# Performance work log

Measured on AMD Instinct MI355X. Metric: run time of the kernel, lower is better.

## Reference

```python
import jax, jax.numpy as jnp
import numpy as np

D_MODEL = 1024
H = 16
D_K = D_MODEL // H
B, S = 4, 2048
NEG = -1000000000.0


def setup_inputs() -> dict:
    key = jax.random.key(0)
    ks = jax.random.split(key, 12)
    scale = 1.0 / np.sqrt(D_MODEL)
    inp = {
        "query": jax.random.normal(ks[0], (B, S, D_MODEL), jnp.float32),
        "key": jax.random.normal(ks[1], (B, S, D_MODEL), jnp.float32),
        "value": jax.random.normal(ks[2], (B, S, D_MODEL), jnp.float32),
        # causal lower-triangular mask, shape (B, S, S); forward unsqueezes head dim
        "mask": jnp.broadcast_to(jnp.tril(jnp.ones((S, S), jnp.int32)), (B, S, S)),
        "Wq": jax.random.normal(ks[3], (D_MODEL, D_MODEL), jnp.float32) * scale,
        "bq": jnp.zeros((D_MODEL,), jnp.float32),
        "Wk": jax.random.normal(ks[4], (D_MODEL, D_MODEL), jnp.float32) * scale,
        "bk": jnp.zeros((D_MODEL,), jnp.float32),
        "Wv": jax.random.normal(ks[5], (D_MODEL, D_MODEL), jnp.float32) * scale,
        "bv": jnp.zeros((D_MODEL,), jnp.float32),
        "Wo": jax.random.normal(ks[6], (D_MODEL, D_MODEL), jnp.float32) * scale,
        "bo": jnp.zeros((D_MODEL,), jnp.float32),
    }
    return inp


def reference(query, key, value, mask, Wq, bq, Wk, bk, Wv, bv, Wo, bo):
    b, s, _ = query.shape
    # projections (torch Linear: x @ W.T + b); split into heads -> (b, h, s, d_k)
    def proj(x, W, bias):
        return (x @ W.T + bias).reshape(b, -1, H, D_K).transpose(0, 2, 1, 3)

    Q = proj(query, Wq, bq)
    K = proj(key, Wk, bk)
    V = proj(value, Wv, bv)

    scores = jnp.einsum("bhqd,bhkd->bhqk", Q, K) / np.sqrt(D_K)
    m = mask[:, None, :, :]  # (b, 1, s, s)
    scores = jnp.where(m == 0, NEG, scores)
    attn = jax.nn.softmax(scores, axis=-1)
    x = jnp.einsum("bhqk,bhkd->bhqd", attn, V)
    x = x.transpose(0, 2, 1, 3).reshape(b, -1, D_MODEL)
    return x @ Wo.T + bo
```

## Files before the change

### kernel.cpp

```cpp
#include <hip/hip_runtime.h>
#include <hip/hip_bf16.h>

#define DMODEL 1024
#define NH 16
#define DKH 64
#define NB 4
#define SEQ 2048
#define MTOT (NB*SEQ)

typedef __bf16 bf16_t;
typedef __bf16 bf16x8 __attribute__((ext_vector_type(8)));
typedef float f32x4 __attribute__((ext_vector_type(4)));

__device__ __forceinline__ void async_copy16(void* lds, const void* g) {
    __builtin_amdgcn_global_load_lds(
        (const __attribute__((address_space(1))) unsigned int*)g,
        (__attribute__((address_space(3))) unsigned int*)lds, 16, 0, 0);
}

__device__ __forceinline__ float fast_exp2(float x) {
    return __builtin_amdgcn_exp2f(x);
}

__device__ __forceinline__ float rsum16(float v) {
    v += __shfl_xor(v, 1);
    v += __shfl_xor(v, 2);
    v += __shfl_xor(v, 4);
    v += __shfl_xor(v, 8);
    return v;
}

__global__ void cvt_kernel(const float* __restrict__ s0, const float* __restrict__ s1,
                           const float* __restrict__ s2, const float* __restrict__ s3,
                           bf16_t* __restrict__ d0, bf16_t* __restrict__ d1,
                           bf16_t* __restrict__ d2, bf16_t* __restrict__ d3, int n)
{
    const float* s = (blockIdx.y == 0) ? s0 : (blockIdx.y == 1) ? s1 :
                     (blockIdx.y == 2) ? s2 : s3;
    bf16_t* d = (blockIdx.y == 0) ? d0 : (blockIdx.y == 1) ? d1 :
                (blockIdx.y == 2) ? d2 : d3;
    int i = (blockIdx.x * 256 + threadIdx.x) * 8;
    if (i < n) {
        float4 a = *(const float4*)&s[i];
        float4 b = *(const float4*)&s[i + 4];
        union { bf16_t h[8]; uint4 u; } t;
        t.h[0]=(bf16_t)a.x; t.h[1]=(bf16_t)a.y; t.h[2]=(bf16_t)a.z; t.h[3]=(bf16_t)a.w;
        t.h[4]=(bf16_t)b.x; t.h[5]=(bf16_t)b.y; t.h[6]=(bf16_t)b.z; t.h[7]=(bf16_t)b.w;
        *(uint4*)&d[i] = t.u;
    }
}

template<int OUT_MODE>
__global__ __launch_bounds__(256, 3)
void gemm_bt(const bf16_t* __restrict__ A, const bf16_t* __restrict__ W,
             const float* __restrict__ bias, void* __restrict__ out,
             int M, int N, int K, float scale)
{
    __shared__ bf16_t As[128 * 64];
    __shared__ bf16_t Ws[128 * 64];

    const int tid  = threadIdx.x;
    const int wave = tid >> 6;
    const int lane = tid & 63;
    const int ln   = lane & 15;
    const int quad = lane >> 4;
    const int wm   = (wave >> 1) * 64;
    const int wn   = (wave & 1) * 64;
    const int bm   = blockIdx.x * 128;
    const int bn   = blockIdx.y * 128;
    const int srow = wave * 8 + (lane >> 3);
    const int sg   = (lane & 7) * 8;

    f32x4 acc[4][4] = {};

    for (int k0 = 0; k0 < K; k0 += 64) {
        #pragma unroll
        for (int rr = 0; rr < 4; ++rr) {
            int row = rr * 32 + srow;
            async_copy16(&As[(size_t)(rr * 32 + wave * 8) * 64],
                         &A[(size_t)(bm + row) * K + k0 + sg]);
            async_copy16(&Ws[(size_t)(rr * 32 + wave * 8) * 64],
                         &W[(size_t)(bn + row) * K + k0 + sg]);
        }
        __syncthreads();

        bf16x8 af[2][4], wf[2][4];
        #pragma unroll
        for (int h = 0; h < 2; ++h)
            #pragma unroll
            for (int u = 0; u < 4; ++u) {
                af[h][u] = *(const bf16x8*)&As[(wm + u * 16 + ln) * 64 + h * 32 + quad * 8];
                wf[h][u] = *(const bf16x8*)&Ws[(wn + u * 16 + ln) * 64 + h * 32 + quad * 8];
            }
        #pragma unroll
        for (int h = 0; h < 2; ++h)
            #pragma unroll
            for (int im = 0; im < 4; ++im)
                #pragma unroll
                for (int jn = 0; jn < 4; ++jn)
                    acc[im][jn] = __builtin_amdgcn_mfma_f32_16x16x32_bf16(
                        af[h][im], wf[h][jn], acc[im][jn], 0, 0, 0);

        __syncthreads();
    }

    #pragma unroll
    for (int jn = 0; jn < 4; ++jn) {
        int n = bn + wn + jn * 16 + ln;
        float bv = bias[n];
        #pragma unroll
        for (int im = 0; im < 4; ++im) {
            #pragma unroll
            for (int r = 0; r < 4; ++r) {
                int m = bm + wm + im * 16 + quad * 4 + r;
                float v = (acc[im][jn][r] + bv) * scale;
                ((float*)out)[(size_t)m * N + n] = v;
            }
        }
    }
}

__global__ __launch_bounds__(256, 3)
void gemm_qkv(const bf16_t* __restrict__ Aq, const bf16_t* __restrict__ Ak,
              const bf16_t* __restrict__ Av, const bf16_t* __restrict__ W3,
              const float* __restrict__ bqp, const float* __restrict__ bkp,
              const float* __restrict__ bvp,
              bf16_t* __restrict__ Qh, bf16_t* __restrict__ Kh,
              bf16_t* __restrict__ Vth, float qscale)
{
    __shared__ bf16_t As[128 * 64];
    __shared__ bf16_t Ws[128 * 64];

    const int K    = DMODEL;
    const int tid  = threadIdx.x;
    const int wave = tid >> 6;
    const int lane = tid & 63;
    const int ln   = lane & 15;
    const int quad = lane >> 4;
    const int wm   = (wave >> 1) * 64;
    const int wn   = (wave & 1) * 64;
    const int bm   = blockIdx.x * 128;
    const int bnG  = blockIdx.y * 128;
    const int sel  = blockIdx.y >> 3;
    const bf16_t* A = (sel == 0) ? Aq : (sel == 1) ? Ak : Av;
    const int srow = wave * 8 + (lane >> 3);
    const int sg   = (lane & 7) * 8;

    f32x4 acc[4][4] = {};

    for (int k0 = 0; k0 < K; k0 += 64) {
        #pragma unroll
        for (int rr = 0; rr < 4; ++rr) {
            int row = rr * 32 + srow;
            async_copy16(&As[(size_t)(rr * 32 + wave * 8) * 64],
                         &A[(size_t)(bm + row) * K + k0 + sg]);
            async_copy16(&Ws[(size_t)(rr * 32 + wave * 8) * 64],
                         &W3[(size_t)(bnG + row) * K + k0 + sg]);
        }
        __syncthreads();

        bf16x8 af[2][4], wf[2][4];
        #pragma unroll
        for (int h = 0; h < 2; ++h)
            #pragma unroll
            for (int u = 0; u < 4; ++u) {
                af[h][u] = *(const bf16x8*)&As[(wm + u * 16 + ln) * 64 + h * 32 + quad * 8];
                wf[h][u] = *(const bf16x8*)&Ws[(wn + u * 16 + ln) * 64 + h * 32 + quad * 8];
            }
        #pragma unroll
        for (int h = 0; h < 2; ++h)
            #pragma unroll
            for (int im = 0; im < 4; ++im)
                #pragma unroll
                for (int jn = 0; jn < 4; ++jn)
                    acc[im][jn] = __builtin_amdgcn_mfma_f32_16x16x32_bf16(
                        af[h][im], wf[h][jn], acc[im][jn], 0, 0, 0);

        __syncthreads();
    }

    const float* bias = (sel == 0) ? bqp : (sel == 1) ? bkp : bvp;
    const float scale = (sel == 0) ? qscale : 1.0f;
    const int bn = bnG & (DMODEL - 1);

    #pragma unroll
    for (int jn = 0; jn < 4; ++jn) {
        int n = bn + wn + jn * 16 + ln;
        float bv = bias[n];
        int h = n >> 6, d = n & 63;
        #pragma unroll
        for (int im = 0; im < 4; ++im) {
            #pragma unroll
            for (int r = 0; r < 4; ++r) {
                int m = bm + wm + im * 16 + quad * 4 + r;
                float v = (acc[im][jn][r] + bv) * scale;
                int b = m >> 11, s = m & (SEQ - 1);
                if (sel == 2) {
                    Vth[(((size_t)(b * NH + h)) * DKH + d) * SEQ + s] = (bf16_t)v;
                } else {
                    bf16_t* outp = (sel == 1) ? Kh : Qh;
                    outp[(((size_t)(b * NH + h)) * SEQ + s) * DKH + d] = (bf16_t)v;
                }
            }
        }
    }
}

__global__ __launch_bounds__(256, 2)
void attn_kernel(const bf16_t* __restrict__ Q, const bf16_t* __restrict__ Km,
                 const bf16_t* __restrict__ Vt, bf16_t* __restrict__ X)
{
    __shared__ __align__(16) bf16_t Ks[2][64 * 64];
    __shared__ __align__(16) bf16_t Vs[2][64 * 64];
    __shared__ __align__(16) bf16_t Ps[4][32][72];

    const int tid  = threadIdx.x;
    const int wave = tid >> 6;
    const int lane = tid & 63;
    const int ln   = lane & 15;
    const int quad = lane >> 4;
    const int cs   = ln & 7;

    const int bh  = blockIdx.x;
    const int qtA = blockIdx.y;
    const int qtB = 15 - qtA;
    const int q0A = qtA * 128;
    const int q0B = qtB * 128;
    const size_t base = (size_t)bh * SEQ * DKH;

    bf16x8 aq[4][2];
    #pragma unroll
    for (int st = 0; st < 4; ++st) {
        const int sb = ((st < 2) ? q0A : q0B) + (st & 1) * 64;
        const bf16_t* qr = Q + base + (size_t)(sb + wave * 16 + ln) * DKH;
        aq[st][0] = *(const bf16x8*)(qr + quad * 8);
        aq[st][1] = *(const bf16x8*)(qr + 32 + quad * 8);
    }

    f32x4 oacc[4][4] = {};
    float psum[4][4] = {};

    const int nkt = 2 * qtB + 2;

    const int srow8 = lane >> 3;
    const int schk  = lane & 7;

    #pragma unroll
    for (int qq = 0; qq < 2; ++qq) {
        const int rb  = wave * 16 + qq * 8;
        const int row = rb + srow8;
        const int csr = schk ^ (row & 7);
        async_copy16(&Ks[0][rb * 64], Km + base + (size_t)row * DKH + csr * 8);
        async_copy16(&Vs[0][rb * 64], Vt + base + (size_t)row * SEQ + csr * 8);
    }
    __syncthreads();

    int cur = 0;
    for (int kt = 0; kt < nkt; ++kt, cur ^= 1) {
        const int j0 = kt * 64;

        if (kt + 1 < nkt) {
            const int jn0 = j0 + 64;
            #pragma unroll
            for (int qq = 0; qq < 2; ++qq) {
                const int rb  = wave * 16 + qq * 8;
                const int row = rb + srow8;
                const int csr = schk ^ (row & 7);
                async_copy16(&Ks[cur ^ 1][rb * 64],
                             Km + base + (size_t)(jn0 + row) * DKH + csr * 8);
                async_copy16(&Vs[cur ^ 1][rb * 64],
                             Vt + base + (size_t)row * SEQ + jn0 + csr * 8);
            }
        }

        bf16x8 kf[4][2];
        #pragma unroll
        for (int jn = 0; jn < 4; ++jn) {
            const int rr = (jn * 16 + ln) * 64;
            kf[jn][0] = *(const bf16x8*)&Ks[cur][rr + ((quad    ) ^ cs) * 8];
            kf[jn][1] = *(const bf16x8*)&Ks[cur][rr + ((4 + quad) ^ cs) * 8];
        }
        bf16x8 vf[4][2];
        #pragma unroll
        for (int nj = 0; nj < 4; ++nj) {
            const int rr = (nj * 16 + ln) * 64;
            vf[nj][0] = *(const bf16x8*)&Vs[cur][rr + ((quad    ) ^ cs) * 8];
            vf[nj][1] = *(const bf16x8*)&Vs[cur][rr + ((4 + quad) ^ cs) * 8];
        }

        #pragma unroll
        for (int pair = 0; pair < 2; ++pair) {
            const int q0p = (pair == 0) ? q0A : q0B;

            f32x4 s[2][4] = {};
            #pragma unroll
            for (int sl = 0; sl < 2; ++sl) {
                const int st = pair * 2 + sl;
                const int sb = q0p + sl * 64;
                if (j0 > sb + 63) continue;
                #pragma unroll
                for (int jn = 0; jn < 4; ++jn) {
                    s[sl][jn] = __builtin_amdgcn_mfma_f32_16x16x32_bf16(aq[st][0], kf[jn][0], s[sl][jn], 0, 0, 0);
                    s[sl][jn] = __builtin_amdgcn_mfma_f32_16x16x32_bf16(aq[st][1], kf[jn][1], s[sl][jn], 0, 0, 0);
                }
            }

            #pragma unroll
            for (int sl = 0; sl < 2; ++sl) {
                const int st = pair * 2 + sl;
                const int sb = q0p + sl * 64;
                if (j0 > sb + 63) continue;
                const int rbase = sb + wave * 16 + quad * 4;
                const bool diag = (j0 + 63 > sb);
                #pragma unroll
                for (int r = 0; r < 4; ++r) {
                    float rowsum = 0.f;
                    #pragma unroll
                    for (int jn = 0; jn < 4; ++jn) {
                        float v = s[sl][jn][r];
                        if (diag) {
                            int col = j0 + jn * 16 + ln;
                            if (col > rbase + r) v = -1e30f;
                        }
                        float p = fast_exp2(v);
                        s[sl][jn][r] = p;
                        rowsum += p;
                    }
                    psum[st][r] += rowsum;
                }
                #pragma unroll
                for (int r = 0; r < 4; ++r)
                    #pragma unroll
                    for (int jn = 0; jn < 4; ++jn)
                        Ps[wave][sl * 16 + quad * 4 + r][jn * 16 + ln] = (bf16_t)s[sl][jn][r];

                bf16x8 ap0 = *(const bf16x8*)&Ps[wave][sl * 16 + ln][quad * 8];
                bf16x8 ap1 = *(const bf16x8*)&Ps[wave][sl * 16 + ln][32 + quad * 8];
                #pragma unroll
                for (int nj = 0; nj < 4; ++nj) {
                    oacc[st][nj] = __builtin_amdgcn_mfma_f32_16x16x32_bf16(ap0, vf[nj][0], oacc[st][nj], 0, 0, 0);
                    oacc[st][nj] = __builtin_amdgcn_mfma_f32_16x16x32_bf16(ap1, vf[nj][1], oacc[st][nj], 0, 0, 0);
                }
            }
        }

        __syncthreads();
    }

    const int bb = bh >> 4, hh = bh & 15;
    #pragma unroll
    for (int st = 0; st < 4; ++st) {
        const int sb = ((st < 2) ? q0A : q0B) + (st & 1) * 64;
        #pragma unroll
        for (int r = 0; r < 4; ++r) {
            int sg = sb + wave * 16 + quad * 4 + r;
            float inv = 1.f / rsum16(psum[st][r]);
            #pragma unroll
            for (int nj = 0; nj < 4; ++nj)
                X[((size_t)(bb * SEQ + sg)) * DMODEL + hh * DKH + nj * 16 + ln] =
                    (bf16_t)(oacc[st][nj][r] * inv);
        }
    }
}

extern "C" void kernel_launch(void* const* d_in, const int* in_sizes, int n_in,
                              void* d_out, int out_size, void* d_ws, size_t ws_size,
                              hipStream_t stream)
{
    const float* query = (const float*)d_in[0];
    const float* key   = (const float*)d_in[1];
    const float* value = (const float*)d_in[2];
    const float* Wq = (const float*)d_in[4];
    const float* bq = (const float*)d_in[5];
    const float* Wk = (const float*)d_in[6];
    const float* bk = (const float*)d_in[7];
    const float* Wv = (const float*)d_in[8];
    const float* bv = (const float*)d_in[9];
    const float* Wo = (const float*)d_in[10];
    const float* bo = (const float*)d_in[11];
    float* out = (float*)d_out;

    char* ws = (char*)d_ws;
    bf16_t* qb  = (bf16_t*)(ws);
    bf16_t* kb  = (bf16_t*)(ws + ((size_t)16 << 20));
    bf16_t* vb  = (bf16_t*)(ws + ((size_t)32 << 20));
    bf16_t* Qh  = (bf16_t*)(ws + ((size_t)48 << 20));
    bf16_t* Wqb = (bf16_t*)(ws + ((size_t)64 << 20));
    bf16_t* Wkb = (bf16_t*)(ws + ((size_t)66 << 20));
    bf16_t* Wvb = (bf16_t*)(ws + ((size_t)68 << 20));
    bf16_t* Wob = (bf16_t*)(ws + ((size_t)70 << 20));
    bf16_t* Kh  = (bf16_t*)d_out;
    bf16_t* Vth = (bf16_t*)((char*)d_out + ((size_t)16 << 20));
    bf16_t* X   = qb;

    const int nAct = MTOT * DMODEL;
    const int nW   = DMODEL * DMODEL;
    cvt_kernel<<<dim3(nAct / 2048, 3), 256, 0, stream>>>(query, key, value, query,
                                                         qb, kb, vb, qb, nAct);
    cvt_kernel<<<dim3(nW / 2048, 4), 256, 0, stream>>>(Wq, Wk, Wv, Wo,
                                                       Wqb, Wkb, Wvb, Wob, nW);

    dim3 bt(256);
    const float qscale = 0.125f * 1.4426950408889634f;

    gemm_qkv<<<dim3(MTOT / 128, 3 * DMODEL / 128), bt, 0, stream>>>(
        qb, kb, vb, Wqb, bq, bk, bv, Qh, Kh, Vth, qscale);

    attn_kernel<<<dim3(NB * NH, SEQ / 256), bt, 0, stream>>>(Qh, Kh, Vth, X);

    gemm_bt<1><<<dim3(MTOT / 128, DMODEL / 128), bt, 0, stream>>>(
        X, Wob, bo, out, MTOT, DMODEL, DMODEL, 1.0f);
}
```

Measured before the change: 374.3 us.

## Enlarge QKV GEMM tile to 256x128 with 8 waves and XOR-swizzled LDS

The QKV projection GEMM now uses 512-thread blocks covering 256 rows by 128 columns, so each weight tile loaded into LDS is shared by twice as many rows. The LDS layout adds an XOR swizzle on 16-byte chunks to avoid bank conflicts when fragments are read for MFMA. In the attention kernel, the P-matrix stores for both sub-tiles are split into a separate loop from the P·V MFMA loop, to let the LDS writes and reads batch together. The trade-off is more LDS per block, a different occupancy bound, and half as many QKV blocks in the grid.

```diff
diff --git a/kernel.cpp b/kernel.cpp
--- a/kernel.cpp
+++ b/kernel.cpp
@@ -120,7 +120,7 @@
     }
 }
 
-__global__ __launch_bounds__(256, 3)
+__global__ __launch_bounds__(512, 2)
 void gemm_qkv(const bf16_t* __restrict__ Aq, const bf16_t* __restrict__ Ak,
               const bf16_t* __restrict__ Av, const bf16_t* __restrict__ W3,
               const float* __restrict__ bqp, const float* __restrict__ bkp,
@@ -128,8 +128,8 @@
               bf16_t* __restrict__ Qh, bf16_t* __restrict__ Kh,
               bf16_t* __restrict__ Vth, float qscale)
 {
-    __shared__ bf16_t As[128 * 64];
-    __shared__ bf16_t Ws[128 * 64];
+    __shared__ __align__(16) bf16_t As[256 * 64];
+    __shared__ __align__(16) bf16_t Ws[128 * 64];
 
     const int K    = DMODEL;
     const int tid  = threadIdx.x;
@@ -137,25 +137,33 @@
     const int lane = tid & 63;
     const int ln   = lane & 15;
     const int quad = lane >> 4;
-    const int wm   = (wave >> 1) * 64;
-    const int wn   = (wave & 1) * 64;
-    const int bm   = blockIdx.x * 128;
+    const int wr   = wave >> 1;
+    const int wc   = wave & 1;
+    const int cs   = ln & 7;
+    const int bm   = blockIdx.x * 256;
     const int bnG  = blockIdx.y * 128;
     const int sel  = blockIdx.y >> 3;
     const bf16_t* A = (sel == 0) ? Aq : (sel == 1) ? Ak : Av;
-    const int srow = wave * 8 + (lane >> 3);
-    const int sg   = (lane & 7) * 8;
+
+    const int srow8 = tid >> 3;
+    const int schk  = tid & 7;
 
     f32x4 acc[4][4] = {};
 
     for (int k0 = 0; k0 < K; k0 += 64) {
         #pragma unroll
-        for (int rr = 0; rr < 4; ++rr) {
-            int row = rr * 32 + srow;
-            async_copy16(&As[(size_t)(rr * 32 + wave * 8) * 64],
-                         &A[(size_t)(bm + row) * K + k0 + sg]);
-            async_copy16(&Ws[(size_t)(rr * 32 + wave * 8) * 64],
-                         &W3[(size_t)(bnG + row) * K + k0 + sg]);
+        for (int b = 0; b < 4; ++b) {
+            const int row = b * 64 + srow8;
+            const int csr = schk ^ (row & 7);
+            async_copy16(&As[(size_t)(b * 64 + (tid >> 6) * 8) * 64],
+                         &A[(size_t)(bm + row) * K + k0 + csr * 8]);
+        }
+        #pragma unroll
+        for (int b = 0; b < 2; ++b) {
+            const int row = b * 64 + srow8;
+            const int csr = schk ^ (row & 7);
+            async_copy16(&Ws[(size_t)(b * 64 + (tid >> 6) * 8) * 64],
+                         &W3[(size_t)(bnG + row) * K + k0 + csr * 8]);
         }
         __syncthreads();
 
@@ -164,8 +172,10 @@
         for (int h = 0; h < 2; ++h)
             #pragma unroll
             for (int u = 0; u < 4; ++u) {
-                af[h][u] = *(const bf16x8*)&As[(wm + u * 16 + ln) * 64 + h * 32 + quad * 8];
-                wf[h][u] = *(const bf16x8*)&Ws[(wn + u * 16 + ln) * 64 + h * 32 + quad * 8];
+                af[h][u] = *(const bf16x8*)&As[(wr * 64 + u * 16 + ln) * 64 +
+                                               ((h * 4 + quad) ^ cs) * 8];
+                wf[h][u] = *(const bf16x8*)&Ws[(wc * 64 + u * 16 + ln) * 64 +
+                                               ((h * 4 + quad) ^ cs) * 8];
             }
         #pragma unroll
         for (int h = 0; h < 2; ++h)
@@ -185,14 +195,14 @@
 
     #pragma unroll
     for (int jn = 0; jn < 4; ++jn) {
-        int n = bn + wn + jn * 16 + ln;
+        int n = bn + wc * 64 + jn * 16 + ln;
         float bv = bias[n];
         int h = n >> 6, d = n & 63;
         #pragma unroll
         for (int im = 0; im < 4; ++im) {
             #pragma unroll
             for (int r = 0; r < 4; ++r) {
-                int m = bm + wm + im * 16 + quad * 4 + r;
+                int m = bm + wr * 64 + im * 16 + quad * 4 + r;
                 float v = (acc[im][jn][r] + bv) * scale;
                 int b = m >> 11, s = m & (SEQ - 1);
                 if (sel == 2) {
@@ -333,7 +343,13 @@
                     #pragma unroll
                     for (int jn = 0; jn < 4; ++jn)
                         Ps[wave][sl * 16 + quad * 4 + r][jn * 16 + ln] = (bf16_t)s[sl][jn][r];
-
+            }
+
+            #pragma unroll
+            for (int sl = 0; sl < 2; ++sl) {
+                const int st = pair * 2 + sl;
+                const int sb = q0p + sl * 64;
+                if (j0 > sb + 63) continue;
                 bf16x8 ap0 = *(const bf16x8*)&Ps[wave][sl * 16 + ln][quad * 8];
                 bf16x8 ap1 = *(const bf16x8*)&Ps[wave][sl * 16 + ln][32 + quad * 8];
                 #pragma unroll
@@ -400,14 +416,13 @@
     cvt_kernel<<<dim3(nW / 2048, 4), 256, 0, stream>>>(Wq, Wk, Wv, Wo,
                                                        Wqb, Wkb, Wvb, Wob, nW);
 
-    dim3 bt(256);
     const float qscale = 0.125f * 1.4426950408889634f;
 
-    gemm_qkv<<<dim3(MTOT / 128, 3 * DMODEL / 128), bt, 0, stream>>>(
+    gemm_qkv<<<dim3(MTOT / 256, 3 * DMODEL / 128), dim3(512), 0, stream>>>(
         qb, kb, vb, Wqb, bq, bk, bv, Qh, Kh, Vth, qscale);
 
-    attn_kernel<<<dim3(NB * NH, SEQ / 256), bt, 0, stream>>>(Qh, Kh, Vth, X);
-
-    gemm_bt<1><<<dim3(MTOT / 128, DMODEL / 128), bt, 0, stream>>>(
+    attn_kernel<<<dim3(NB * NH, SEQ / 256), dim3(256), 0, stream>>>(Qh, Kh, Vth, X);
+
+    gemm_bt<1><<<dim3(MTOT / 128, DMODEL / 128), dim3(256), 0, stream>>>(
         X, Wob, bo, out, MTOT, DMODEL, DMODEL, 1.0f);
 }
```

Result: no change. 377.6 us (+0.9%).

## Replace projection GEMMs with 256x256 double-buffered, swizzled 8-wave pipelined kernel

Applied to the files above, without the earlier changes.

The QKV and output projection GEMMs move from 128x128 tiles with a single LDS buffer and a full sync each k-step to a 256x256 tile run by 512 threads. The new kernel double-buffers LDS, XOR-swizzles the column layout to avoid bank conflicts, and splits each k-step into four quadrant phases that issue the next tiles' async loads while MFMAs run. It uses setprio and explicit waitcnt/barriers. In attention, the P-to-LDS writes for both sub-tiles now finish before the PV MFMAs read them back. The tradeoff is 128KB of LDS per block, so one block per CU, and fewer blocks for the output GEMM (128).

```diff
diff --git a/kernel.cpp b/kernel.cpp
--- a/kernel.cpp
+++ b/kernel.cpp
@@ -50,156 +50,153 @@
     }
 }
 
-template<int OUT_MODE>
-__global__ __launch_bounds__(256, 3)
-void gemm_bt(const bf16_t* __restrict__ A, const bf16_t* __restrict__ W,
-             const float* __restrict__ bias, void* __restrict__ out,
-             int M, int N, int K, float scale)
-{
-    __shared__ bf16_t As[128 * 64];
-    __shared__ bf16_t Ws[128 * 64];
-
-    const int tid  = threadIdx.x;
-    const int wave = tid >> 6;
-    const int lane = tid & 63;
-    const int ln   = lane & 15;
-    const int quad = lane >> 4;
-    const int wm   = (wave >> 1) * 64;
-    const int wn   = (wave & 1) * 64;
-    const int bm   = blockIdx.x * 128;
-    const int bn   = blockIdx.y * 128;
-    const int srow = wave * 8 + (lane >> 3);
-    const int sg   = (lane & 7) * 8;
-
-    f32x4 acc[4][4] = {};
-
-    for (int k0 = 0; k0 < K; k0 += 64) {
-        #pragma unroll
-        for (int rr = 0; rr < 4; ++rr) {
-            int row = rr * 32 + srow;
-            async_copy16(&As[(size_t)(rr * 32 + wave * 8) * 64],
-                         &A[(size_t)(bm + row) * K + k0 + sg]);
-            async_copy16(&Ws[(size_t)(rr * 32 + wave * 8) * 64],
-                         &W[(size_t)(bn + row) * K + k0 + sg]);
-        }
-        __syncthreads();
-
-        bf16x8 af[2][4], wf[2][4];
-        #pragma unroll
-        for (int h = 0; h < 2; ++h)
-            #pragma unroll
-            for (int u = 0; u < 4; ++u) {
-                af[h][u] = *(const bf16x8*)&As[(wm + u * 16 + ln) * 64 + h * 32 + quad * 8];
-                wf[h][u] = *(const bf16x8*)&Ws[(wn + u * 16 + ln) * 64 + h * 32 + quad * 8];
-            }
-        #pragma unroll
-        for (int h = 0; h < 2; ++h)
-            #pragma unroll
-            for (int im = 0; im < 4; ++im)
+
+__device__ __forceinline__ void stage_half(bf16_t* buf, const bf16_t* Gp,
+                                           int half, int kcol, int tid)
+{
+    const int sr = tid >> 3, sc = tid & 7, wv = tid >> 6;
+    #pragma unroll
+    for (int j = 0; j < 2; ++j) {
+        const int row = half * 128 + j * 64 + sr;
+        async_copy16(&buf[(size_t)(half * 128 + j * 64 + wv * 8) * 64],
+                     Gp + (size_t)row * DMODEL + kcol + ((sc ^ (sr & 7)) * 8));
+    }
+}
+
+template<int PM, int PN, typename STG>
+__device__ __forceinline__ void phase(const bf16_t* Ab, const bf16_t* Bb,
+                                      f32x4 (&accq)[4][2],
+                                      int wave_r, int wave_c, int ln, int quad,
+                                      int cs, STG&& stg)
+{
+    bf16x8 af[4][2], bfv[2][2];
+    #pragma unroll
+    for (int mf = 0; mf < 4; ++mf) {
+        const int ar = PM * 128 + wave_r * 64 + mf * 16 + ln;
+        af[mf][0] = *(const bf16x8*)&Ab[ar * 64 + ((quad    ) ^ cs) * 8];
+        af[mf][1] = *(const bf16x8*)&Ab[ar * 64 + ((4 + quad) ^ cs) * 8];
+    }
+    #pragma unroll
+    for (int nf = 0; nf < 2; ++nf) {
+        const int br = PN * 128 + wave_c * 32 + nf * 16 + ln;
+        bfv[nf][0] = *(const bf16x8*)&Bb[br * 64 + ((quad    ) ^ cs) * 8];
+        bfv[nf][1] = *(const bf16x8*)&Bb[br * 64 + ((4 + quad) ^ cs) * 8];
+    }
+    stg();
+    __builtin_amdgcn_s_barrier();
+    asm volatile("s_waitcnt lgkmcnt(0)" ::: "memory");
+    __builtin_amdgcn_sched_barrier(0);
+    __builtin_amdgcn_s_setprio(1);
+    #pragma unroll
+    for (int mf = 0; mf < 4; ++mf)
+        #pragma unroll
+        for (int nf = 0; nf < 2; ++nf) {
+            accq[mf][nf] = __builtin_amdgcn_mfma_f32_16x16x32_bf16(
+                af[mf][0], bfv[nf][0], accq[mf][nf], 0, 0, 0);
+            accq[mf][nf] = __builtin_amdgcn_mfma_f32_16x16x32_bf16(
+                af[mf][1], bfv[nf][1], accq[mf][nf], 0, 0, 0);
+        }
+    __builtin_amdgcn_s_setprio(0);
+}
+
+template<int MODE>
+__global__ __launch_bounds__(512)
+void gemm8(const bf16_t* __restrict__ Aq, const bf16_t* __restrict__ Ak,
+           const bf16_t* __restrict__ Av, const bf16_t* __restrict__ W,
+           const float* __restrict__ bqp, const float* __restrict__ bkp,
+           const float* __restrict__ bvp,
+           bf16_t* __restrict__ Qh, bf16_t* __restrict__ Kh,
+           bf16_t* __restrict__ Vth, float* __restrict__ fout, float qscale)
+{
+    __shared__ __align__(16) bf16_t Abuf[2][256 * 64];
+    __shared__ __align__(16) bf16_t Bbuf[2][256 * 64];
+
+    const int tid    = threadIdx.x;
+    const int wave   = tid >> 6;
+    const int lane   = tid & 63;
+    const int ln     = lane & 15;
+    const int quad   = lane >> 4;
+    const int cs     = ln & 7;
+    const int wave_r = wave >> 2;
+    const int wave_c = wave & 3;
+    const int bm     = blockIdx.x * 256;
+    const int bnG    = blockIdx.y * 256;
+    const int sel    = (MODE == 0) ? (bnG >> 10) : 0;
+    const bf16_t* A  = (MODE == 1) ? Aq
+                     : ((sel == 0) ? Aq : (sel == 1) ? Ak : Av);
+
+    const bf16_t* Ag = A + (size_t)bm  * DMODEL;
+    const bf16_t* Wg = W + (size_t)bnG * DMODEL;
+
+    f32x4 acc[4][4][2] = {};
+
+    stage_half(Abuf[0], Ag, 0, 0, tid);  stage_half(Abuf[0], Ag, 1, 0, tid);
+    stage_half(Bbuf[0], Wg, 0, 0, tid);  stage_half(Bbuf[0], Wg, 1, 0, tid);
+    stage_half(Abuf[1], Ag, 0, 64, tid); stage_half(Abuf[1], Ag, 1, 64, tid);
+    stage_half(Bbuf[1], Wg, 0, 64, tid); stage_half(Bbuf[1], Wg, 1, 64, tid);
+    asm volatile("s_waitcnt vmcnt(8)" ::: "memory");
+    __builtin_amdgcn_s_barrier();
+
+    const int NT = DMODEL / 64;
+    for (int g = 0; g < NT; ++g) {
+        const int b  = g & 1;
+        const int nb = b ^ 1;
+        const bf16_t* Ab = &Abuf[b][0];
+        const bf16_t* Bb = &Bbuf[b][0];
+
+        phase<0, 0>(Ab, Bb, acc[0], wave_r, wave_c, ln, quad, cs, [&] {
+            if (g >= 1 && g + 1 < NT) stage_half(Abuf[nb], Ag, 1, (g + 1) * 64, tid);
+        });
+        __builtin_amdgcn_s_barrier();
+
+        phase<1, 0>(Ab, Bb, acc[1], wave_r, wave_c, ln, quad, cs, [&] {
+            if (g >= 1 && g + 1 < NT) stage_half(Bbuf[nb], Wg, 1, (g + 1) * 64, tid);
+        });
+        __builtin_amdgcn_s_barrier();
+
+        phase<0, 1>(Ab, Bb, acc[2], wave_r, wave_c, ln, quad, cs, [&] {
+            if (g + 2 < NT) stage_half(Bbuf[b], Wg, 0, (g + 2) * 64, tid);
+        });
+        __builtin_amdgcn_s_barrier();
+
+        phase<1, 1>(Ab, Bb, acc[3], wave_r, wave_c, ln, quad, cs, [&] {
+            if (g + 2 < NT) stage_half(Abuf[b], Ag, 0, (g + 2) * 64, tid);
+        });
+        if (g < NT - 2)       asm volatile("s_waitcnt vmcnt(4)" ::: "memory");
+        else if (g == NT - 2) asm volatile("s_waitcnt vmcnt(0)" ::: "memory");
+        __builtin_amdgcn_s_barrier();
+    }
+
+    const float* bias = (MODE == 1) ? bqp
+                      : ((sel == 0) ? bqp : (sel == 1) ? bkp : bvp);
+    const float scale = (MODE == 0 && sel == 0) ? qscale : 1.0f;
+
+    #pragma unroll
+    for (int q = 0; q < 4; ++q) {
+        const int mh = q & 1, nh = q >> 1;
+        #pragma unroll
+        for (int nf = 0; nf < 2; ++nf) {
+            const int nabs = bnG + nh * 128 + wave_c * 32 + nf * 16 + ln;
+            const int nloc = nabs & (DMODEL - 1);
+            const float bv = bias[nloc];
+            const int h = nloc >> 6, d = nloc & 63;
+            #pragma unroll
+            for (int mf = 0; mf < 4; ++mf) {
                 #pragma unroll
-                for (int jn = 0; jn < 4; ++jn)
-                    acc[im][jn] = __builtin_amdgcn_mfma_f32_16x16x32_bf16(
-                        af[h][im], wf[h][jn], acc[im][jn], 0, 0, 0);
-
-        __syncthreads();
-    }
-
-    #pragma unroll
-    for (int jn = 0; jn < 4; ++jn) {
-        int n = bn + wn + jn * 16 + ln;
-        float bv = bias[n];
-        #pragma unroll
-        for (int im = 0; im < 4; ++im) {
-            #pragma unroll
-            for (int r = 0; r < 4; ++r) {
-                int m = bm + wm + im * 16 + quad * 4 + r;
-                float v = (acc[im][jn][r] + bv) * scale;
-                ((float*)out)[(size_t)m * N + n] = v;
-            }
-        }
-    }
-}
-
-__global__ __launch_bounds__(256, 3)
-void gemm_qkv(const bf16_t* __restrict__ Aq, const bf16_t* __restrict__ Ak,
-              const bf16_t* __restrict__ Av, const bf16_t* __restrict__ W3,
-              const float* __restrict__ bqp, const float* __restrict__ bkp,
-              const float* __restrict__ bvp,
-              bf16_t* __restrict__ Qh, bf16_t* __restrict__ Kh,
-              bf16_t* __restrict__ Vth, float qscale)
-{
-    __shared__ bf16_t As[128 * 64];
-    __shared__ bf16_t Ws[128 * 64];
-
-    const int K    = DMODEL;
-    const int tid  = threadIdx.x;
-    const int wave = tid >> 6;
-    const int lane = tid & 63;
-    const int ln   = lane & 15;
-    const int quad = lane >> 4;
-    const int wm   = (wave >> 1) * 64;
-    const int wn   = (wave & 1) * 64;
-    const int bm   = blockIdx.x * 128;
-    const int bnG  = blockIdx.y * 128;
-    const int sel  = blockIdx.y >> 3;
-    const bf16_t* A = (sel == 0) ? Aq : (sel == 1) ? Ak : Av;
-    const int srow = wave * 8 + (lane >> 3);
-    const int sg   = (lane & 7) * 8;
-
-    f32x4 acc[4][4] = {};
-
-    for (int k0 = 0; k0 < K; k0 += 64) {
-        #pragma unroll
-        for (int rr = 0; rr < 4; ++rr) {
-            int row = rr * 32 + srow;
-            async_copy16(&As[(size_t)(rr * 32 + wave * 8) * 64],
-                         &A[(size_t)(bm + row) * K + k0 + sg]);
-            async_copy16(&Ws[(size_t)(rr * 32 + wave * 8) * 64],
-                         &W3[(size_t)(bnG + row) * K + k0 + sg]);
-        }
-        __syncthreads();
-
-        bf16x8 af[2][4], wf[2][4];
-        #pragma unroll
-        for (int h = 0; h < 2; ++h)
-            #pragma unroll
-            for (int u = 0; u < 4; ++u) {
-                af[h][u] = *(const bf16x8*)&As[(wm + u * 16 + ln) * 64 + h * 32 + quad * 8];
-                wf[h][u] = *(const bf16x8*)&Ws[(wn + u * 16 + ln) * 64 + h * 32 + quad * 8];
-            }
-        #pragma unroll
-        for (int h = 0; h < 2; ++h)
-            #pragma unroll
-            for (int im = 0; im < 4; ++im)
-                #pragma unroll
-                for (int jn = 0; jn < 4; ++jn)
-                    acc[im][jn] = __builtin_amdgcn_mfma_f32_16x16x32_bf16(
-                        af[h][im], wf[h][jn], acc[im][jn], 0, 0, 0);
-
-        __syncthreads();
-    }
-
-    const float* bias = (sel == 0) ? bqp : (sel == 1) ? bkp : bvp;
-    const float scale = (sel == 0) ? qscale : 1.0f;
-    const int bn = bnG & (DMODEL - 1);
-
-    #pragma unroll
-    for (int jn = 0; jn < 4; ++jn) {
-        int n = bn + wn + jn * 16 + ln;
-        float bv = bias[n];
-        int h = n >> 6, d = n & 63;
-        #pragma unroll
-        for (int im = 0; im < 4; ++im) {
-            #pragma unroll
-            for (int r = 0; r < 4; ++r) {
-                int m = bm + wm + im * 16 + quad * 4 + r;
-                float v = (acc[im][jn][r] + bv) * scale;
-                int b = m >> 11, s = m & (SEQ - 1);
-                if (sel == 2) {
-                    Vth[(((size_t)(b * NH + h)) * DKH + d) * SEQ + s] = (bf16_t)v;
-                } else {
-                    bf16_t* outp = (sel == 1) ? Kh : Qh;
-                    outp[(((size_t)(b * NH + h)) * SEQ + s) * DKH + d] = (bf16_t)v;
+                for (int r = 0; r < 4; ++r) {
+                    const int m = bm + mh * 128 + wave_r * 64 + mf * 16 + quad * 4 + r;
+                    const float v = (acc[q][mf][nf][r] + bv) * scale;
+                    if (MODE == 1) {
+                        fout[(size_t)m * DMODEL + nloc] = v;
+                    } else {
+                        const int bb = m >> 11, s = m & (SEQ - 1);
+                        if (sel == 2) {
+                            Vth[(((size_t)(bb * NH + h)) * DKH + d) * SEQ + s] = (bf16_t)v;
+                        } else {
+                            bf16_t* outp = (sel == 1) ? Kh : Qh;
+                            outp[(((size_t)(bb * NH + h)) * SEQ + s) * DKH + d] = (bf16_t)v;
+                        }
+                    }
                 }
             }
         }
@@ -333,7 +330,13 @@
                     #pragma unroll
                     for (int jn = 0; jn < 4; ++jn)
                         Ps[wave][sl * 16 + quad * 4 + r][jn * 16 + ln] = (bf16_t)s[sl][jn][r];
-
+            }
+
+            #pragma unroll
+            for (int sl = 0; sl < 2; ++sl) {
+                const int st = pair * 2 + sl;
+                const int sb = q0p + sl * 64;
+                if (j0 > sb + 63) continue;
                 bf16x8 ap0 = *(const bf16x8*)&Ps[wave][sl * 16 + ln][quad * 8];
                 bf16x8 ap1 = *(const bf16x8*)&Ps[wave][sl * 16 + ln][32 + quad * 8];
                 #pragma unroll
@@ -400,14 +403,13 @@
     cvt_kernel<<<dim3(nW / 2048, 4), 256, 0, stream>>>(Wq, Wk, Wv, Wo,
                                                        Wqb, Wkb, Wvb, Wob, nW);
 
-    dim3 bt(256);
     const float qscale = 0.125f * 1.4426950408889634f;
 
-    gemm_qkv<<<dim3(MTOT / 128, 3 * DMODEL / 128), bt, 0, stream>>>(
-        qb, kb, vb, Wqb, bq, bk, bv, Qh, Kh, Vth, qscale);
-
-    attn_kernel<<<dim3(NB * NH, SEQ / 256), bt, 0, stream>>>(Qh, Kh, Vth, X);
-
-    gemm_bt<1><<<dim3(MTOT / 128, DMODEL / 128), bt, 0, stream>>>(
-        X, Wob, bo, out, MTOT, DMODEL, DMODEL, 1.0f);
-}
+    gemm8<0><<<dim3(MTOT / 256, 3 * DMODEL / 256), dim3(512), 0, stream>>>(
+        qb, kb, vb, Wqb, bq, bk, bv, Qh, Kh, Vth, nullptr, qscale);
+
+    attn_kernel<<<dim3(NB * NH, SEQ / 256), dim3(256), 0, stream>>>(Qh, Kh, Vth, X);
+
+    gemm8<1><<<dim3(MTOT / 256, DMODEL / 256), dim3(512), 0, stream>>>(
+        X, X, X, Wob, bo, bo, bo, nullptr, nullptr, nullptr, out, 1.0f);
+}
```

Result: slower. 401.3 us (+7.2%).

## Fuse fp32-to-bf16 activation conversion into QKV GEMM and retile output GEMM

Applied to the files above, without the earlier changes.

The separate conversion pass over query/key/value is removed. The QKV GEMM now loads fp32 activations straight into LDS with an XOR swizzle and converts them to bf16 while building MFMA fragments. This avoids writing and re-reading three 16M-element bf16 buffers, but doubles the A-tile LDS footprint and global read bytes inside the GEMM and adds conversion ALU work. The output projection gets its own 64x128-tile kernel with higher occupancy, which doubles the block count for better CU fill.

```diff
diff --git a/kernel.cpp b/kernel.cpp
--- a/kernel.cpp
+++ b/kernel.cpp
@@ -50,88 +50,17 @@
     }
 }
 
-template<int OUT_MODE>
 __global__ __launch_bounds__(256, 3)
-void gemm_bt(const bf16_t* __restrict__ A, const bf16_t* __restrict__ W,
-             const float* __restrict__ bias, void* __restrict__ out,
-             int M, int N, int K, float scale)
-{
-    __shared__ bf16_t As[128 * 64];
-    __shared__ bf16_t Ws[128 * 64];
-
-    const int tid  = threadIdx.x;
-    const int wave = tid >> 6;
-    const int lane = tid & 63;
-    const int ln   = lane & 15;
-    const int quad = lane >> 4;
-    const int wm   = (wave >> 1) * 64;
-    const int wn   = (wave & 1) * 64;
-    const int bm   = blockIdx.x * 128;
-    const int bn   = blockIdx.y * 128;
-    const int srow = wave * 8 + (lane >> 3);
-    const int sg   = (lane & 7) * 8;
-
-    f32x4 acc[4][4] = {};
-
-    for (int k0 = 0; k0 < K; k0 += 64) {
-        #pragma unroll
-        for (int rr = 0; rr < 4; ++rr) {
-            int row = rr * 32 + srow;
-            async_copy16(&As[(size_t)(rr * 32 + wave * 8) * 64],
-                         &A[(size_t)(bm + row) * K + k0 + sg]);
-            async_copy16(&Ws[(size_t)(rr * 32 + wave * 8) * 64],
-                         &W[(size_t)(bn + row) * K + k0 + sg]);
-        }
-        __syncthreads();
-
-        bf16x8 af[2][4], wf[2][4];
-        #pragma unroll
-        for (int h = 0; h < 2; ++h)
-            #pragma unroll
-            for (int u = 0; u < 4; ++u) {
-                af[h][u] = *(const bf16x8*)&As[(wm + u * 16 + ln) * 64 + h * 32 + quad * 8];
-                wf[h][u] = *(const bf16x8*)&Ws[(wn + u * 16 + ln) * 64 + h * 32 + quad * 8];
-            }
-        #pragma unroll
-        for (int h = 0; h < 2; ++h)
-            #pragma unroll
-            for (int im = 0; im < 4; ++im)
-                #pragma unroll
-                for (int jn = 0; jn < 4; ++jn)
-                    acc[im][jn] = __builtin_amdgcn_mfma_f32_16x16x32_bf16(
-                        af[h][im], wf[h][jn], acc[im][jn], 0, 0, 0);
-
-        __syncthreads();
-    }
-
-    #pragma unroll
-    for (int jn = 0; jn < 4; ++jn) {
-        int n = bn + wn + jn * 16 + ln;
-        float bv = bias[n];
-        #pragma unroll
-        for (int im = 0; im < 4; ++im) {
-            #pragma unroll
-            for (int r = 0; r < 4; ++r) {
-                int m = bm + wm + im * 16 + quad * 4 + r;
-                float v = (acc[im][jn][r] + bv) * scale;
-                ((float*)out)[(size_t)m * N + n] = v;
-            }
-        }
-    }
-}
-
-__global__ __launch_bounds__(256, 3)
-void gemm_qkv(const bf16_t* __restrict__ Aq, const bf16_t* __restrict__ Ak,
-              const bf16_t* __restrict__ Av, const bf16_t* __restrict__ W3,
+void gemm_qkv(const float* __restrict__ Aq, const float* __restrict__ Ak,
+              const float* __restrict__ Av, const bf16_t* __restrict__ W3,
               const float* __restrict__ bqp, const float* __restrict__ bkp,
               const float* __restrict__ bvp,
               bf16_t* __restrict__ Qh, bf16_t* __restrict__ Kh,
               bf16_t* __restrict__ Vth, float qscale)
 {
-    __shared__ bf16_t As[128 * 64];
-    __shared__ bf16_t Ws[128 * 64];
-
-    const int K    = DMODEL;
+    __shared__ __align__(16) float  Asf[128 * 64];
+    __shared__ __align__(16) bf16_t Ws[128 * 64];
+
     const int tid  = threadIdx.x;
     const int wave = tid >> 6;
     const int lane = tid & 63;
@@ -142,40 +71,56 @@
     const int bm   = blockIdx.x * 128;
     const int bnG  = blockIdx.y * 128;
     const int sel  = blockIdx.y >> 3;
-    const bf16_t* A = (sel == 0) ? Aq : (sel == 1) ? Ak : Av;
+    const float* A32 = (sel == 0) ? Aq : (sel == 1) ? Ak : Av;
     const int srow = wave * 8 + (lane >> 3);
     const int sg   = (lane & 7) * 8;
+    const int ar16 = tid >> 4;
+    const int ac16 = tid & 15;
 
     f32x4 acc[4][4] = {};
 
-    for (int k0 = 0; k0 < K; k0 += 64) {
+    for (int k0 = 0; k0 < DMODEL; k0 += 64) {
+        #pragma unroll
+        for (int b = 0; b < 8; ++b) {
+            const int row = b * 16 + ar16;
+            const int csr = ac16 ^ (row & 15);
+            async_copy16(&Asf[(size_t)(b * 16 + wave * 4) * 64],
+                         &A32[(size_t)(bm + row) * DMODEL + k0 + csr * 4]);
+        }
         #pragma unroll
         for (int rr = 0; rr < 4; ++rr) {
-            int row = rr * 32 + srow;
-            async_copy16(&As[(size_t)(rr * 32 + wave * 8) * 64],
-                         &A[(size_t)(bm + row) * K + k0 + sg]);
+            const int row = rr * 32 + srow;
             async_copy16(&Ws[(size_t)(rr * 32 + wave * 8) * 64],
-                         &W3[(size_t)(bnG + row) * K + k0 + sg]);
+                         &W3[(size_t)(bnG + row) * DMODEL + k0 + sg]);
         }
         __syncthreads();
 
-        bf16x8 af[2][4], wf[2][4];
-        #pragma unroll
-        for (int h = 0; h < 2; ++h)
+        #pragma unroll
+        for (int h = 0; h < 2; ++h) {
+            bf16x8 af[4], wf[4];
             #pragma unroll
             for (int u = 0; u < 4; ++u) {
-                af[h][u] = *(const bf16x8*)&As[(wm + u * 16 + ln) * 64 + h * 32 + quad * 8];
-                wf[h][u] = *(const bf16x8*)&Ws[(wn + u * 16 + ln) * 64 + h * 32 + quad * 8];
-            }
-        #pragma unroll
-        for (int h = 0; h < 2; ++h)
+                const int row = wm + u * 16 + ln;
+                const int swz = row & 15;
+                const int c0  = (h * 8 + quad * 2)     ^ swz;
+                const int c1  = (h * 8 + quad * 2 + 1) ^ swz;
+                f32x4 p0 = *(const f32x4*)&Asf[row * 64 + c0 * 4];
+                f32x4 p1 = *(const f32x4*)&Asf[row * 64 + c1 * 4];
+                bf16x8 t;
+                t[0] = (bf16_t)p0[0]; t[1] = (bf16_t)p0[1];
+                t[2] = (bf16_t)p0[2]; t[3] = (bf16_t)p0[3];
+                t[4] = (bf16_t)p1[0]; t[5] = (bf16_t)p1[1];
+                t[6] = (bf16_t)p1[2]; t[7] = (bf16_t)p1[3];
+                af[u] = t;
+                wf[u] = *(const bf16x8*)&Ws[(wn + u * 16 + ln) * 64 + h * 32 + quad * 8];
+            }
             #pragma unroll
             for (int im = 0; im < 4; ++im)
                 #pragma unroll
                 for (int jn = 0; jn < 4; ++jn)
                     acc[im][jn] = __builtin_amdgcn_mfma_f32_16x16x32_bf16(
-                        af[h][im], wf[h][jn], acc[im][jn], 0, 0, 0);
-
+                        af[im], wf[jn], acc[im][jn], 0, 0, 0);
+        }
         __syncthreads();
     }
 
@@ -201,6 +146,81 @@
                     bf16_t* outp = (sel == 1) ? Kh : Qh;
                     outp[(((size_t)(b * NH + h)) * SEQ + s) * DKH + d] = (bf16_t)v;
                 }
+            }
+        }
+    }
+}
+
+__global__ __launch_bounds__(256, 4)
+void gemm_o(const bf16_t* __restrict__ A, const bf16_t* __restrict__ W,
+            const float* __restrict__ bias, float* __restrict__ out)
+{
+    __shared__ bf16_t As[64 * 64];
+    __shared__ bf16_t Ws[128 * 64];
+
+    const int tid  = threadIdx.x;
+    const int wave = tid >> 6;
+    const int lane = tid & 63;
+    const int ln   = lane & 15;
+    const int quad = lane >> 4;
+    const int wm   = (wave >> 1) * 32;
+    const int wn   = (wave & 1) * 64;
+    const int bm   = blockIdx.x * 64;
+    const int bn   = blockIdx.y * 128;
+    const int ar   = tid >> 3;
+    const int ac   = (tid & 7) * 8;
+    const int srow = wave * 8 + (lane >> 3);
+    const int sg   = (lane & 7) * 8;
+
+    f32x4 acc[2][4] = {};
+
+    for (int k0 = 0; k0 < DMODEL; k0 += 64) {
+        #pragma unroll
+        for (int b2 = 0; b2 < 2; ++b2) {
+            const int row = b2 * 32 + ar;
+            async_copy16(&As[(size_t)(b2 * 32 + wave * 8) * 64],
+                         &A[(size_t)(bm + row) * DMODEL + k0 + ac]);
+        }
+        #pragma unroll
+        for (int rr = 0; rr < 4; ++rr) {
+            const int row = rr * 32 + srow;
+            async_copy16(&Ws[(size_t)(rr * 32 + wave * 8) * 64],
+                         &W[(size_t)(bn + row) * DMODEL + k0 + sg]);
+        }
+        __syncthreads();
+
+        bf16x8 af[2][2], wf[2][4];
+        #pragma unroll
+        for (int h = 0; h < 2; ++h) {
+            #pragma unroll
+            for (int u = 0; u < 2; ++u)
+                af[h][u] = *(const bf16x8*)&As[(wm + u * 16 + ln) * 64 + h * 32 + quad * 8];
+            #pragma unroll
+            for (int u = 0; u < 4; ++u)
+                wf[h][u] = *(const bf16x8*)&Ws[(wn + u * 16 + ln) * 64 + h * 32 + quad * 8];
+        }
+        #pragma unroll
+        for (int h = 0; h < 2; ++h)
+            #pragma unroll
+            for (int im = 0; im < 2; ++im)
+                #pragma unroll
+                for (int jn = 0; jn < 4; ++jn)
+                    acc[im][jn] = __builtin_amdgcn_mfma_f32_16x16x32_bf16(
+                        af[h][im], wf[h][jn], acc[im][jn], 0, 0, 0);
+
+        __syncthreads();
+    }
+
+    #pragma unroll
+    for (int jn = 0; jn < 4; ++jn) {
+        const int n = bn + wn + jn * 16 + ln;
+        const float bv = bias[n];
+        #pragma unroll
+        for (int im = 0; im < 2; ++im) {
+            #pragma unroll
+            for (int r = 0; r < 4; ++r) {
+                const int m = bm + wm + im * 16 + quad * 4 + r;
+                out[(size_t)m * DMODEL + n] = acc[im][jn][r] + bv;
             }
         }
     }
@@ -381,9 +401,7 @@
     float* out = (float*)d_out;
 
     char* ws = (char*)d_ws;
-    bf16_t* qb  = (bf16_t*)(ws);
-    bf16_t* kb  = (bf16_t*)(ws + ((size_t)16 << 20));
-    bf16_t* vb  = (bf16_t*)(ws + ((size_t)32 << 20));
+    bf16_t* X   = (bf16_t*)(ws);
     bf16_t* Qh  = (bf16_t*)(ws + ((size_t)48 << 20));
     bf16_t* Wqb = (bf16_t*)(ws + ((size_t)64 << 20));
     bf16_t* Wkb = (bf16_t*)(ws + ((size_t)66 << 20));
@@ -391,12 +409,8 @@
     bf16_t* Wob = (bf16_t*)(ws + ((size_t)70 << 20));
     bf16_t* Kh  = (bf16_t*)d_out;
     bf16_t* Vth = (bf16_t*)((char*)d_out + ((size_t)16 << 20));
-    bf16_t* X   = qb;
-
-    const int nAct = MTOT * DMODEL;
-    const int nW   = DMODEL * DMODEL;
-    cvt_kernel<<<dim3(nAct / 2048, 3), 256, 0, stream>>>(query, key, value, query,
-                                                         qb, kb, vb, qb, nAct);
+
+    const int nW = DMODEL * DMODEL;
     cvt_kernel<<<dim3(nW / 2048, 4), 256, 0, stream>>>(Wq, Wk, Wv, Wo,
                                                        Wqb, Wkb, Wvb, Wob, nW);
 
@@ -404,10 +418,9 @@
     const float qscale = 0.125f * 1.4426950408889634f;
 
     gemm_qkv<<<dim3(MTOT / 128, 3 * DMODEL / 128), bt, 0, stream>>>(
-        qb, kb, vb, Wqb, bq, bk, bv, Qh, Kh, Vth, qscale);
+        query, key, value, Wqb, bq, bk, bv, Qh, Kh, Vth, qscale);
 
     attn_kernel<<<dim3(NB * NH, SEQ / 256), bt, 0, stream>>>(Qh, Kh, Vth, X);
 
-    gemm_bt<1><<<dim3(MTOT / 128, DMODEL / 128), bt, 0, stream>>>(
-        X, Wob, bo, out, MTOT, DMODEL, DMODEL, 1.0f);
-}
+    gemm_o<<<dim3(MTOT / 64, DMODEL / 128), bt, 0, stream>>>(X, Wob, bo, out);
+}
```

Result: no change. 371.8 us (-0.7%).
